# Kernel optimization log

Hardware: AMD Instinct MI355X
Metric: run time of the kernel (lower is better)

Reference implementation:

```python
import jax, jax.numpy as jnp
import numpy as np

N_NODES = 50000
N_EDGES = 800000
N_GRAPHS = 64
NFEAT, NHID, NHEADS, NCLASS = 128, 64, 4, 1
NLAYERS = 3
DT, ALPHA, GAMMA = 1.0, 1.0, 1.0
NEG_SLOPE = 0.2  # PyG GATConv default


def setup_inputs() -> dict:
    key = jax.random.key(0)
    ks = jax.random.split(key, 16)
    HW = NHEADS * NHID
    s = 0.05
    return {
        "x": jax.random.normal(ks[0], (N_NODES, 125), jnp.float32),
        "pos": jax.random.normal(ks[1], (N_NODES, 3), jnp.float32),
        "edge_index": jax.random.randint(ks[2], (2, N_EDGES), 0, N_NODES, jnp.int64),
        "batch": jnp.sort(jax.random.randint(ks[3], (N_NODES,), 0, N_GRAPHS, jnp.int64)),
        "enc_w": jax.random.normal(ks[4], (NFEAT, NHID), jnp.float32) * s,
        "enc_b": jnp.zeros((NHID,), jnp.float32),
        "res_w": jax.random.normal(ks[5], (NHID, HW), jnp.float32) * s,
        "res_b": jnp.zeros((HW,), jnp.float32),
        "lin_w": jax.random.normal(ks[6], (NHID, HW), jnp.float32) * s,
        "att_src": jax.random.normal(ks[7], (NHEADS, NHID), jnp.float32) * s,
        "att_dst": jax.random.normal(ks[8], (NHEADS, NHID), jnp.float32) * s,
        "conv_b": jnp.zeros((HW,), jnp.float32),
        "dec_w": jax.random.normal(ks[9], (NHID, NCLASS), jnp.float32) * s,
        "dec_b": jnp.zeros((NCLASS,), jnp.float32),
    }


def gat_conv(X, src, dst, lin_w, att_src, att_dst, conv_b):
    # X: [N, NHID] -> h: [N, H, C]; per-edge attention, segment softmax over dst, scatter-add
    N = X.shape[0]
    h = (X @ lin_w).reshape(N, NHEADS, NHID)
    a_src = jnp.einsum("nhc,hc->nh", h, att_src)  # [N, H]
    a_dst = jnp.einsum("nhc,hc->nh", h, att_dst)
    e = jax.nn.leaky_relu(a_src[src] + a_dst[dst], NEG_SLOPE)  # [E, H]
    m = jax.ops.segment_max(e, dst, num_segments=N)
    e = jnp.exp(e - m[dst])
    z = jax.ops.segment_sum(e, dst, num_segments=N)
    att = e / z[dst]  # [E, H] (self-loops guarantee z > 0)
    msg = h[src] * att[:, :, None]  # [E, H, C]
    out = jax.ops.segment_sum(msg, dst, num_segments=N)  # [N, H, C]
    return out.reshape(N, NHEADS * NHID) + conv_b


def reference(x, pos, edge_index, batch, enc_w, enc_b, res_w, res_b,
              lin_w, att_src, att_dst, conv_b, dec_w, dec_b):
    inp = jnp.concatenate([x, pos], axis=-1)  # [N, NFEAT]
    N = inp.shape[0]
    loop = jnp.arange(N, dtype=edge_index.dtype)
    src = jnp.concatenate([edge_index[0], loop])  # add self loops (PyG default)
    dst = jnp.concatenate([edge_index[1], loop])

    Y = inp @ enc_w + enc_b
    X = Y
    for _ in range(NLAYERS):
        conv_out = gat_conv(X, src, dst, lin_w, att_src, att_dst, conv_b)
        res = X @ res_w + res_b
        # NB: faithful to torch .view(n, -1, nheads).mean(-1) head-mixing reshape
        mixed = jax.nn.elu(conv_out + res).reshape(N, -1, NHEADS).mean(axis=-1)
        Y = Y + DT * (mixed - ALPHA * Y - GAMMA * X)
        X = X + DT * Y
    X = X @ dec_w + dec_b  # [N, NCLASS]
    pooled = jax.ops.segment_sum(X, batch, num_segments=N_GRAPHS)  # [G, NCLASS]
    return pooled.squeeze(-1)
```

## Files before the change

kernel.cpp:

```cpp
#include <hip/hip_runtime.h>
#include <hip/hip_bf16.h>

#define N_NODES  50000
#define N_EDGES  800000
#define E_TOT    850000
#define N_GRAPHS 64
#define NHID     64
#define NHEADS   4
#define HW       256
#define NEG_SLOPE 0.2f
#define DEC_BLOCKS 512
#define LOG_NPB  32
#define ENC_NPB  32
#define SCAN_NB  ((N_NODES + 255) / 256)
#define MFMA_NPB 64

typedef __attribute__((ext_vector_type(8))) short bf16x8;
typedef __attribute__((ext_vector_type(4))) float f32x4;

__device__ __forceinline__ float bf2f(unsigned short u) {
    return __uint_as_float(((unsigned)u) << 16);
}
__device__ __forceinline__ unsigned short f2bf(float f) {
    __hip_bfloat16 h = __float2bfloat16(f);
    return *reinterpret_cast<unsigned short*>(&h);
}
__device__ __forceinline__ float lrelu(float v) {
    return (v > 0.f) ? v : NEG_SLOPE * v;
}

__global__ __launch_bounds__(256) void encoder_kernel(
        const float* __restrict__ x, const float* __restrict__ pos,
        const float* __restrict__ enc_w, const float* __restrict__ enc_b,
        float* __restrict__ Y, float* __restrict__ X) {
    __shared__ float ws[128 * 64];
    __shared__ float xs[ENC_NPB][128];
    int t = threadIdx.x;
    int base = blockIdx.x * ENC_NPB;
    int nx = min(ENC_NPB, N_NODES - base);
    for (int i = t; i < 128 * 64; i += 256) ws[i] = enc_w[i];
    for (int i = t; i < nx * 125; i += 256) {
        int nn = i / 125, k = i - nn * 125;
        xs[nn][k] = x[(size_t)base * 125 + i];
    }
    for (int i = t; i < nx * 3; i += 256) {
        int nn = i / 3, k = i - nn * 3;
        xs[nn][125 + k] = pos[(size_t)(base + nn) * 3 + k];
    }
    __syncthreads();
    int c = t & 63, wv = t >> 6;
    float bias = enc_b[c];
    for (int nn = wv; nn < nx; nn += 4) {
        float acc = bias;
        #pragma unroll 16
        for (int k = 0; k < 128; ++k) acc += xs[nn][k] * ws[k * 64 + c];
        int n = base + nn;
        Y[n * 64 + c] = acc;
        X[n * 64 + c] = acc;
    }
}

__global__ void hist_kernel(const int* __restrict__ ei, int* __restrict__ counts) {
    int e = blockIdx.x * blockDim.x + threadIdx.x;
    if (e >= E_TOT) return;
    int d = (e < N_EDGES) ? ei[N_EDGES + e] : (e - N_EDGES);
    atomicAdd(&counts[d], 1);
}

__global__ __launch_bounds__(256) void scan_reduce_kernel(const int* __restrict__ counts,
                                                          int* __restrict__ bsum) {
    __shared__ int s[256];
    int t = threadIdx.x;
    int i = blockIdx.x * 256 + t;
    s[t] = (i < N_NODES) ? counts[i] : 0;
    __syncthreads();
    #pragma unroll
    for (int off = 128; off >= 1; off >>= 1) {
        if (t < off) s[t] += s[t + off];
        __syncthreads();
    }
    if (t == 0) bsum[blockIdx.x] = s[0];
}

__global__ __launch_bounds__(256) void scan_bsum_kernel(const int* __restrict__ bsum,
                                                        int* __restrict__ boff) {
    __shared__ int a[256];
    int t = threadIdx.x;
    int v = (t < SCAN_NB) ? bsum[t] : 0;
    a[t] = v;
    __syncthreads();
    #pragma unroll
    for (int off = 1; off < 256; off <<= 1) {
        int u = (t >= off) ? a[t - off] : 0;
        __syncthreads();
        a[t] += u;
        __syncthreads();
    }
    if (t < SCAN_NB) boff[t] = a[t] - v;
}

__global__ __launch_bounds__(256) void scan_write_kernel(const int* __restrict__ counts,
                                                         const int* __restrict__ boff,
                                                         int* __restrict__ row_ptr,
                                                         int* __restrict__ cursor) {
    __shared__ int a[256];
    int t = threadIdx.x;
    int i = blockIdx.x * 256 + t;
    int v = (i < N_NODES) ? counts[i] : 0;
    a[t] = v;
    __syncthreads();
    #pragma unroll
    for (int off = 1; off < 256; off <<= 1) {
        int u = (t >= off) ? a[t - off] : 0;
        __syncthreads();
        a[t] += u;
        __syncthreads();
    }
    if (i < N_NODES) {
        int ex = boff[blockIdx.x] + a[t] - v;
        row_ptr[i] = ex;
        cursor[i]  = ex;
        if (i == N_NODES - 1) row_ptr[N_NODES] = E_TOT;
    }
}

__global__ void scatter_kernel(const int* __restrict__ ei, int* __restrict__ cursor,
                               int* __restrict__ col) {
    int e = blockIdx.x * blockDim.x + threadIdx.x;
    if (e >= E_TOT) return;
    int s, d;
    if (e < N_EDGES) { s = ei[e]; d = ei[N_EDGES + e]; }
    else             { s = d = e - N_EDGES; }
    int pos = atomicAdd(&cursor[d], 1);
    col[pos] = s;
}

__global__ __launch_bounds__(256) void wa_precompute_kernel(
        const float* __restrict__ lin_w, const float* __restrict__ att_src,
        const float* __restrict__ att_dst, float* __restrict__ wa) {
    int t = threadIdx.x;
    int k = t >> 2, head = t & 3;
    float s = 0.f, d = 0.f;
    #pragma unroll 8
    for (int c = 0; c < 64; ++c) {
        float lw = lin_w[k * 256 + head * 64 + c];
        s += lw * att_src[head * 64 + c];
        d += lw * att_dst[head * 64 + c];
    }
    wa[k * 8 + head]     = s;
    wa[k * 8 + 4 + head] = d;
}

__global__ __launch_bounds__(256) void prep_wt_kernel(
        const float* __restrict__ lin_w, const float* __restrict__ res_w,
        unsigned short* __restrict__ Wt) {
    int k = blockIdx.x;
    int t = threadIdx.x;
    Wt[(size_t)t * 64 + k]         = f2bf(lin_w[k * 256 + t]);
    Wt[(size_t)(t + 256) * 64 + k] = f2bf(res_w[k * 256 + t]);
}

__global__ __launch_bounds__(256) void logit_kernel(
        const float* __restrict__ X, const float* __restrict__ wa,
        float* __restrict__ a_src, float* __restrict__ a_dst) {
    __shared__ float was[64 * 8];
    __shared__ float xs[LOG_NPB * 68];
    int t = threadIdx.x;
    int base = blockIdx.x * LOG_NPB;
    int nx = min(LOG_NPB, N_NODES - base);
    for (int i = t; i < 512; i += 256) was[i] = wa[i];
    for (int i = t; i < nx * 64; i += 256)
        xs[(i >> 6) * 68 + (i & 63)] = X[(size_t)base * 64 + i];
    __syncthreads();
    int sub = t >> 3, out = t & 7;
    if (sub >= nx) return;
    float acc = 0.f;
    #pragma unroll 8
    for (int k = 0; k < 64; ++k) acc += xs[sub * 68 + k] * was[k * 8 + out];
    int n = base + sub;
    if (out < 4) a_src[n * 4 + out] = acc;
    else         a_dst[n * 4 + (out - 4)] = acc;
}

__global__ __launch_bounds__(256) void lin_mfma_kernel(
        const float* __restrict__ X, const unsigned short* __restrict__ Wt,
        __hip_bfloat16* __restrict__ h, __hip_bfloat16* __restrict__ res) {
    __shared__ unsigned short As[64 * 64];
    __shared__ unsigned short Bs[256 * 64];
    int t = threadIdx.x;
    int lane = t & 63, w = t >> 6;
    int base = blockIdx.x * MFMA_NPB;

    for (int i = 0; i < 4; ++i) {
        int chunk = i * 256 + t;
        int row = chunk >> 4, q = chunk & 15;
        int node = base + row;
        float4 xv = make_float4(0.f, 0.f, 0.f, 0.f);
        if (node < N_NODES) xv = ((const float4*)X)[(size_t)node * 16 + q];
        ushort4 b;
        b.x = f2bf(xv.x); b.y = f2bf(xv.y); b.z = f2bf(xv.z); b.w = f2bf(xv.w);
        int idx = row * 64 + ((q * 4) ^ ((row & 7) << 3));
        *(ushort4*)&As[idx] = b;
    }

    int rowl = (w << 4) + (lane & 15);
    int kg   = (lane >> 4) << 3;
    int amask = (lane & 7) << 3;
    bf16x8 af0, af1;

    for (int p = 0; p < 2; ++p) {
        __syncthreads();
        const unsigned short* Wp = Wt + (size_t)p * 256 * 64;
        for (int i = 0; i < 8; ++i) {
            int chunk = i * 256 + t;
            int n = chunk >> 3, c = chunk & 7;
            int idx = n * 64 + ((c * 8) ^ ((n & 7) << 3));
            *(uint4*)&Bs[idx] = *(const uint4*)(Wp + chunk * 8);
        }
        __syncthreads();
        if (p == 0) {
            af0 = *(bf16x8*)&As[rowl * 64 + (kg ^ amask)];
            af1 = *(bf16x8*)&As[rowl * 64 + ((32 + kg) ^ amask)];
        }
        for (int ct = 0; ct < 16; ++ct) {
            int coll = (ct << 4) + (lane & 15);
            bf16x8 bf0 = *(bf16x8*)&Bs[coll * 64 + (kg ^ amask)];
            bf16x8 bf1 = *(bf16x8*)&Bs[coll * 64 + ((32 + kg) ^ amask)];
            f32x4 acc = {0.f, 0.f, 0.f, 0.f};
            acc = __builtin_amdgcn_mfma_f32_16x16x32_bf16(af0, bf0, acc, 0, 0, 0);
            acc = __builtin_amdgcn_mfma_f32_16x16x32_bf16(af1, bf1, acc, 0, 0, 0);
            int rowbase = base + (w << 4) + ((lane >> 4) << 2);
            #pragma unroll
            for (int r = 0; r < 4; ++r) {
                int rn = rowbase + r;
                if (rn < N_NODES) {
                    if (p == 0) h[(size_t)rn * 256 + coll] = __float2bfloat16(acc[r]);
                    else        res[(size_t)rn * 256 + coll] = __float2bfloat16(acc[r]);
                }
            }
        }
    }
}

__global__ __launch_bounds__(256) void fused_gat_kernel(
        const int* __restrict__ rp, const int* __restrict__ col,
        const float* __restrict__ a_src, const float* __restrict__ a_dst,
        const __hip_bfloat16* __restrict__ h,
        const float* __restrict__ conv_b,
        const __hip_bfloat16* __restrict__ res,
        float* __restrict__ Y, float* __restrict__ X) {
    __shared__ float satt[4][64][4];
    __shared__ int   scol[4][64];
    int n = (blockIdx.x * blockDim.x + threadIdx.x) >> 6;
    if (n >= N_NODES) return;
    int lane = threadIdx.x & 63;
    int w = (threadIdx.x >> 6) & 3;
    int head = lane >> 4;
    int base = rp[n];
    int deg  = rp[n + 1] - base;
    const ushort* hp = (const ushort*)h;
    float4 ad = ((const float4*)a_dst)[n];

    float a0 = 0.f, a1 = 0.f, a2 = 0.f, a3 = 0.f;

    if (deg <= 64) {
        int s = 0;
        float l0 = -3.0e38f, l1 = -3.0e38f, l2 = -3.0e38f, l3 = -3.0e38f;
        if (lane < deg) {
            s = col[base + lane];
            float4 as = ((const float4*)a_src)[s];
            l0 = lrelu(as.x + ad.x); l1 = lrelu(as.y + ad.y);
            l2 = lrelu(as.z + ad.z); l3 = lrelu(as.w + ad.w);
        }
        float m0 = l0, m1 = l1, m2 = l2, m3 = l3;
        #pragma unroll
        for (int off = 1; off < 64; off <<= 1) {
            m0 = fmaxf(m0, __shfl_xor(m0, off)); m1 = fmaxf(m1, __shfl_xor(m1, off));
            m2 = fmaxf(m2, __shfl_xor(m2, off)); m3 = fmaxf(m3, __shfl_xor(m3, off));
        }
        float e0 = (lane < deg) ? __expf(l0 - m0) : 0.f;
        float e1 = (lane < deg) ? __expf(l1 - m1) : 0.f;
        float e2 = (lane < deg) ? __expf(l2 - m2) : 0.f;
        float e3 = (lane < deg) ? __expf(l3 - m3) : 0.f;
        float z0 = e0, z1 = e1, z2 = e2, z3 = e3;
        #pragma unroll
        for (int off = 1; off < 64; off <<= 1) {
            z0 += __shfl_xor(z0, off); z1 += __shfl_xor(z1, off);
            z2 += __shfl_xor(z2, off); z3 += __shfl_xor(z3, off);
        }
        satt[w][lane][0] = e0 / z0; satt[w][lane][1] = e1 / z1;
        satt[w][lane][2] = e2 / z2; satt[w][lane][3] = e3 / z3;
        scol[w][lane] = s;

        int j = 0;
        for (; j + 2 <= deg; j += 2) {
            int   s0 = scol[w][j],        s1 = scol[w][j + 1];
            float w0 = satt[w][j][head],  w1 = satt[w][j + 1][head];
            ushort4 v0 = *(const ushort4*)(hp + (size_t)s0 * 256 + lane * 4);
            ushort4 v1 = *(const ushort4*)(hp + (size_t)s1 * 256 + lane * 4);
            a0 += w0 * bf2f(v0.x) + w1 * bf2f(v1.x);
            a1 += w0 * bf2f(v0.y) + w1 * bf2f(v1.y);
            a2 += w0 * bf2f(v0.z) + w1 * bf2f(v1.z);
            a3 += w0 * bf2f(v0.w) + w1 * bf2f(v1.w);
        }
        if (j < deg) {
            int   s0 = scol[w][j];
            float w0 = satt[w][j][head];
            ushort4 v0 = *(const ushort4*)(hp + (size_t)s0 * 256 + lane * 4);
            a0 += w0 * bf2f(v0.x); a1 += w0 * bf2f(v0.y);
            a2 += w0 * bf2f(v0.z); a3 += w0 * bf2f(v0.w);
        }
    } else {
        float m0 = -3.0e38f, m1 = -3.0e38f, m2 = -3.0e38f, m3 = -3.0e38f;
        float z0 = 0.f, z1 = 0.f, z2 = 0.f, z3 = 0.f;
        for (int c0 = 0; c0 < deg; c0 += 64) {
            int j = c0 + lane;
            float l0 = -3.0e38f, l1 = -3.0e38f, l2 = -3.0e38f, l3 = -3.0e38f;
            if (j < deg) {
                int s = col[base + j];
                float4 as = ((const float4*)a_src)[s];
                l0 = lrelu(as.x + ad.x); l1 = lrelu(as.y + ad.y);
                l2 = lrelu(as.z + ad.z); l3 = lrelu(as.w + ad.w);
            }
            float c0m = l0, c1m = l1, c2m = l2, c3m = l3;
            #pragma unroll
            for (int off = 1; off < 64; off <<= 1) {
                c0m = fmaxf(c0m, __shfl_xor(c0m, off)); c1m = fmaxf(c1m, __shfl_xor(c1m, off));
                c2m = fmaxf(c2m, __shfl_xor(c2m, off)); c3m = fmaxf(c3m, __shfl_xor(c3m, off));
            }
            float n0 = fmaxf(m0, c0m), n1 = fmaxf(m1, c1m);
            float n2 = fmaxf(m2, c2m), n3 = fmaxf(m3, c3m);
            z0 *= __expf(m0 - n0); z1 *= __expf(m1 - n1);
            z2 *= __expf(m2 - n2); z3 *= __expf(m3 - n3);
            m0 = n0; m1 = n1; m2 = n2; m3 = n3;
            float e0 = (j < deg) ? __expf(l0 - m0) : 0.f;
            float e1 = (j < deg) ? __expf(l1 - m1) : 0.f;
            float e2 = (j < deg) ? __expf(l2 - m2) : 0.f;
            float e3 = (j < deg) ? __expf(l3 - m3) : 0.f;
            #pragma unroll
            for (int off = 1; off < 64; off <<= 1) {
                e0 += __shfl_xor(e0, off); e1 += __shfl_xor(e1, off);
                e2 += __shfl_xor(e2, off); e3 += __shfl_xor(e3, off);
            }
            z0 += e0; z1 += e1; z2 += e2; z3 += e3;
        }
        for (int c0 = 0; c0 < deg; c0 += 64) {
            int j = c0 + lane;
            int s = 0;
            float e0 = 0.f, e1 = 0.f, e2 = 0.f, e3 = 0.f;
            if (j < deg) {
                s = col[base + j];
                float4 as = ((const float4*)a_src)[s];
                e0 = __expf(lrelu(as.x + ad.x) - m0) / z0;
                e1 = __expf(lrelu(as.y + ad.y) - m1) / z1;
                e2 = __expf(lrelu(as.z + ad.z) - m2) / z2;
                e3 = __expf(lrelu(as.w + ad.w) - m3) / z3;
            }
            satt[w][lane][0] = e0; satt[w][lane][1] = e1;
            satt[w][lane][2] = e2; satt[w][lane][3] = e3;
            scol[w][lane] = s;
            int cnt = min(64, deg - c0);
            for (int jj = 0; jj < cnt; ++jj) {
                int   sj = scol[w][jj];
                float ww = satt[w][jj][head];
                ushort4 v = *(const ushort4*)(hp + (size_t)sj * 256 + lane * 4);
                a0 += ww * bf2f(v.x); a1 += ww * bf2f(v.y);
                a2 += ww * bf2f(v.z); a3 += ww * bf2f(v.w);
            }
        }
    }

    ushort4 rr4 = ((const ushort4*)res)[(size_t)n * 64 + lane];
    float4 cb = ((const float4*)conv_b)[lane];
    float v0 = a0 + cb.x + bf2f(rr4.x), v1 = a1 + cb.y + bf2f(rr4.y);
    float v2 = a2 + cb.z + bf2f(rr4.z), v3 = a3 + cb.w + bf2f(rr4.w);
    v0 = (v0 > 0.f) ? v0 : (__expf(v0) - 1.f);
    v1 = (v1 > 0.f) ? v1 : (__expf(v1) - 1.f);
    v2 = (v2 > 0.f) ? v2 : (__expf(v2) - 1.f);
    v3 = (v3 > 0.f) ? v3 : (__expf(v3) - 1.f);
    float mixed = 0.25f * (v0 + v1 + v2 + v3);

    float xv = X[n * 64 + lane];
    float y = Y[n * 64 + lane];
    y  = y + (mixed - y - xv);
    xv = xv + y;
    Y[n * 64 + lane] = y;
    X[n * 64 + lane] = xv;
}

__global__ void decoder_partial_kernel(const float* __restrict__ X, const float* __restrict__ dec_w,
                                       const float* __restrict__ dec_b, const int* __restrict__ batch,
                                       float* __restrict__ partials) {
    __shared__ float sg[N_GRAPHS];
    int t = threadIdx.x;
    if (t < N_GRAPHS) sg[t] = 0.f;
    __syncthreads();
    int lane = t & 63;
    int wave = t >> 6;
    const int npb = (N_NODES + DEC_BLOCKS - 1) / DEC_BLOCKS;
    int start = blockIdx.x * npb;
    int end   = min(start + npb, N_NODES);
    float dw = dec_w[lane];
    float db = dec_b[0];
    for (int n = start + wave; n < end; n += 4) {
        float p = X[n * 64 + lane] * dw;
        #pragma unroll
        for (int off = 32; off >= 1; off >>= 1) p += __shfl_down(p, off);
        if (lane == 0) atomicAdd(&sg[batch[n]], p + db);
    }
    __syncthreads();
    if (t < N_GRAPHS) partials[blockIdx.x * N_GRAPHS + t] = sg[t];
}

__global__ void decoder_reduce_kernel(const float* __restrict__ partials, float* __restrict__ out) {
    __shared__ float red[256];
    int t = threadIdx.x;
    int g = t & 63, j = t >> 6;
    float s = 0.f;
    for (int b = j * (DEC_BLOCKS / 4); b < (j + 1) * (DEC_BLOCKS / 4); ++b)
        s += partials[b * N_GRAPHS + g];
    red[t] = s;
    __syncthreads();
    if (t < 64) out[g] = red[g] + red[64 + g] + red[128 + g] + red[192 + g];
}

extern "C" void kernel_launch(void* const* d_in, const int* in_sizes, int n_in,
                              void* d_out, int out_size, void* d_ws, size_t ws_size,
                              hipStream_t stream) {
    const float* x       = (const float*)d_in[0];
    const float* pos     = (const float*)d_in[1];
    const int*   ei      = (const int*)d_in[2];
    const int*   batch   = (const int*)d_in[3];
    const float* enc_w   = (const float*)d_in[4];
    const float* enc_b   = (const float*)d_in[5];
    const float* res_w   = (const float*)d_in[6];
    const float* res_b   = (const float*)d_in[7];
    const float* lin_w   = (const float*)d_in[8];
    const float* att_src = (const float*)d_in[9];
    const float* att_dst = (const float*)d_in[10];
    const float* conv_b  = (const float*)d_in[11];
    const float* dec_w   = (const float*)d_in[12];
    const float* dec_b   = (const float*)d_in[13];
    float* out = (float*)d_out;

    char* ws = (char*)d_ws;
    size_t off = 0;
    auto alloc = [&](size_t bytes) -> void* {
        void* p = ws + off;
        off += (bytes + 255) & ~size_t(255);
        return p;
    };
    float* Y       = (float*)alloc((size_t)N_NODES * 64 * sizeof(float));
    float* X       = (float*)alloc((size_t)N_NODES * 64 * sizeof(float));
    __hip_bfloat16* h   = (__hip_bfloat16*)alloc((size_t)N_NODES * HW * sizeof(__hip_bfloat16));
    __hip_bfloat16* res = (__hip_bfloat16*)alloc((size_t)N_NODES * HW * sizeof(__hip_bfloat16));
    float* a_src   = (float*)alloc((size_t)N_NODES * NHEADS * sizeof(float));
    float* a_dst   = (float*)alloc((size_t)N_NODES * NHEADS * sizeof(float));
    float* wa      = (float*)alloc((size_t)64 * 8 * sizeof(float));
    unsigned short* Wt = (unsigned short*)alloc((size_t)512 * 64 * sizeof(unsigned short));
    float* partials= (float*)alloc((size_t)DEC_BLOCKS * N_GRAPHS * sizeof(float));
    int*   counts  = (int*)alloc((size_t)N_NODES * sizeof(int));
    int*   row_ptr = (int*)alloc((size_t)(N_NODES + 1) * sizeof(int));
    int*   cursor  = (int*)alloc((size_t)N_NODES * sizeof(int));
    int*   col     = (int*)alloc((size_t)E_TOT * sizeof(int));
    int*   bsum    = (int*)alloc((size_t)SCAN_NB * sizeof(int));
    int*   boff    = (int*)alloc((size_t)SCAN_NB * sizeof(int));

    hipMemsetAsync(counts, 0, (size_t)N_NODES * sizeof(int), stream);
    const int eb = (E_TOT + 255) / 256;
    hist_kernel<<<eb, 256, 0, stream>>>(ei, counts);
    scan_reduce_kernel<<<SCAN_NB, 256, 0, stream>>>(counts, bsum);
    scan_bsum_kernel<<<1, 256, 0, stream>>>(bsum, boff);
    scan_write_kernel<<<SCAN_NB, 256, 0, stream>>>(counts, boff, row_ptr, cursor);
    scatter_kernel<<<eb, 256, 0, stream>>>(ei, cursor, col);

    wa_precompute_kernel<<<1, 256, 0, stream>>>(lin_w, att_src, att_dst, wa);
    prep_wt_kernel<<<64, 256, 0, stream>>>(lin_w, res_w, Wt);
    encoder_kernel<<<(N_NODES + ENC_NPB - 1) / ENC_NPB, 256, 0, stream>>>(
        x, pos, enc_w, enc_b, Y, X);

    const int ab = (N_NODES * 64 + 255) / 256;
    const int mb = (N_NODES + MFMA_NPB - 1) / MFMA_NPB;
    const int gb = (N_NODES + LOG_NPB - 1) / LOG_NPB;
    for (int layer = 0; layer < 3; ++layer) {
        lin_mfma_kernel<<<mb, 256, 0, stream>>>(X, Wt, h, res);
        logit_kernel<<<gb, 256, 0, stream>>>(X, wa, a_src, a_dst);
        fused_gat_kernel<<<ab, 256, 0, stream>>>(row_ptr, col, a_src, a_dst, h,
                                                 conv_b, res, Y, X);
    }

    decoder_partial_kernel<<<DEC_BLOCKS, 256, 0, stream>>>(X, dec_w, dec_b, batch, partials);
    decoder_reduce_kernel<<<1, 256, 0, stream>>>(partials, out);
}
```

Measured before the change: 527.4 us.

## Fuse attention logit projection into MFMA linear kernel and unroll gather by four

```diff
diff --git a/kernel.cpp b/kernel.cpp
--- a/kernel.cpp
+++ b/kernel.cpp
@@ -10,7 +10,6 @@
 #define HW       256
 #define NEG_SLOPE 0.2f
 #define DEC_BLOCKS 512
-#define LOG_NPB  32
 #define ENC_NPB  32
 #define SCAN_NB  ((N_NODES + 255) / 256)
 #define MFMA_NPB 64
@@ -137,7 +136,7 @@
 
 __global__ __launch_bounds__(256) void wa_precompute_kernel(
         const float* __restrict__ lin_w, const float* __restrict__ att_src,
-        const float* __restrict__ att_dst, float* __restrict__ wa) {
+        const float* __restrict__ att_dst, unsigned short* __restrict__ Wt) {
     int t = threadIdx.x;
     int k = t >> 2, head = t & 3;
     float s = 0.f, d = 0.f;
@@ -147,8 +146,10 @@
         s += lw * att_src[head * 64 + c];
         d += lw * att_dst[head * 64 + c];
     }
-    wa[k * 8 + head]     = s;
-    wa[k * 8 + 4 + head] = d;
+    Wt[(size_t)(512 + head) * 64 + k] = f2bf(s);
+    Wt[(size_t)(516 + head) * 64 + k] = f2bf(d);
+    Wt[(size_t)520 * 64 + t]       = 0;
+    Wt[(size_t)520 * 64 + 256 + t] = 0;
 }
 
 __global__ __launch_bounds__(256) void prep_wt_kernel(
@@ -160,31 +161,10 @@
     Wt[(size_t)(t + 256) * 64 + k] = f2bf(res_w[k * 256 + t]);
 }
 
-__global__ __launch_bounds__(256) void logit_kernel(
-        const float* __restrict__ X, const float* __restrict__ wa,
-        float* __restrict__ a_src, float* __restrict__ a_dst) {
-    __shared__ float was[64 * 8];
-    __shared__ float xs[LOG_NPB * 68];
-    int t = threadIdx.x;
-    int base = blockIdx.x * LOG_NPB;
-    int nx = min(LOG_NPB, N_NODES - base);
-    for (int i = t; i < 512; i += 256) was[i] = wa[i];
-    for (int i = t; i < nx * 64; i += 256)
-        xs[(i >> 6) * 68 + (i & 63)] = X[(size_t)base * 64 + i];
-    __syncthreads();
-    int sub = t >> 3, out = t & 7;
-    if (sub >= nx) return;
-    float acc = 0.f;
-    #pragma unroll 8
-    for (int k = 0; k < 64; ++k) acc += xs[sub * 68 + k] * was[k * 8 + out];
-    int n = base + sub;
-    if (out < 4) a_src[n * 4 + out] = acc;
-    else         a_dst[n * 4 + (out - 4)] = acc;
-}
-
 __global__ __launch_bounds__(256) void lin_mfma_kernel(
         const float* __restrict__ X, const unsigned short* __restrict__ Wt,
-        __hip_bfloat16* __restrict__ h, __hip_bfloat16* __restrict__ res) {
+        __hip_bfloat16* __restrict__ h, __hip_bfloat16* __restrict__ res,
+        float* __restrict__ a_src, float* __restrict__ a_dst) {
     __shared__ unsigned short As[64 * 64];
     __shared__ unsigned short Bs[256 * 64];
     int t = threadIdx.x;
@@ -216,6 +196,11 @@
             int n = chunk >> 3, c = chunk & 7;
             int idx = n * 64 + ((c * 8) ^ ((n & 7) << 3));
             *(uint4*)&Bs[idx] = *(const uint4*)(Wp + chunk * 8);
+        }
+        if (p == 1 && t < 128) {
+            int n = t >> 3, c = t & 7;
+            int idx = n * 64 + ((c * 8) ^ ((n & 7) << 3));
+            *(uint4*)&As[idx] = *(const uint4*)(Wt + (size_t)(512 + n) * 64 + c * 8);
         }
         __syncthreads();
         if (p == 0) {
@@ -236,6 +221,23 @@
                 if (rn < N_NODES) {
                     if (p == 0) h[(size_t)rn * 256 + coll] = __float2bfloat16(acc[r]);
                     else        res[(size_t)rn * 256 + coll] = __float2bfloat16(acc[r]);
+                }
+            }
+        }
+        if (p == 1) {
+            int coll = lane & 15;
+            bf16x8 bf0 = *(bf16x8*)&As[coll * 64 + (kg ^ amask)];
+            bf16x8 bf1 = *(bf16x8*)&As[coll * 64 + ((32 + kg) ^ amask)];
+            f32x4 acc = {0.f, 0.f, 0.f, 0.f};
+            acc = __builtin_amdgcn_mfma_f32_16x16x32_bf16(af0, bf0, acc, 0, 0, 0);
+            acc = __builtin_amdgcn_mfma_f32_16x16x32_bf16(af1, bf1, acc, 0, 0, 0);
+            int rowbase = base + (w << 4) + ((lane >> 4) << 2);
+            #pragma unroll
+            for (int r = 0; r < 4; ++r) {
+                int rn = rowbase + r;
+                if (rn < N_NODES) {
+                    if (coll < 4)      a_src[rn * 4 + coll] = acc[r];
+                    else if (coll < 8) a_dst[rn * 4 + (coll - 4)] = acc[r];
                 }
             }
         }
@@ -293,17 +295,21 @@
         scol[w][lane] = s;
 
         int j = 0;
-        for (; j + 2 <= deg; j += 2) {
-            int   s0 = scol[w][j],        s1 = scol[w][j + 1];
-            float w0 = satt[w][j][head],  w1 = satt[w][j + 1][head];
+        for (; j + 4 <= deg; j += 4) {
+            int   s0 = scol[w][j],       s1 = scol[w][j + 1];
+            int   s2 = scol[w][j + 2],   s3 = scol[w][j + 3];
+            float w0 = satt[w][j][head], w1 = satt[w][j + 1][head];
+            float w2 = satt[w][j + 2][head], w3 = satt[w][j + 3][head];
             ushort4 v0 = *(const ushort4*)(hp + (size_t)s0 * 256 + lane * 4);
             ushort4 v1 = *(const ushort4*)(hp + (size_t)s1 * 256 + lane * 4);
-            a0 += w0 * bf2f(v0.x) + w1 * bf2f(v1.x);
-            a1 += w0 * bf2f(v0.y) + w1 * bf2f(v1.y);
-            a2 += w0 * bf2f(v0.z) + w1 * bf2f(v1.z);
-            a3 += w0 * bf2f(v0.w) + w1 * bf2f(v1.w);
-        }
-        if (j < deg) {
+            ushort4 v2 = *(const ushort4*)(hp + (size_t)s2 * 256 + lane * 4);
+            ushort4 v3 = *(const ushort4*)(hp + (size_t)s3 * 256 + lane * 4);
+            a0 += w0 * bf2f(v0.x) + w1 * bf2f(v1.x) + w2 * bf2f(v2.x) + w3 * bf2f(v3.x);
+            a1 += w0 * bf2f(v0.y) + w1 * bf2f(v1.y) + w2 * bf2f(v2.y) + w3 * bf2f(v3.y);
+            a2 += w0 * bf2f(v0.z) + w1 * bf2f(v1.z) + w2 * bf2f(v2.z) + w3 * bf2f(v3.z);
+            a3 += w0 * bf2f(v0.w) + w1 * bf2f(v1.w) + w2 * bf2f(v2.w) + w3 * bf2f(v3.w);
+        }
+        for (; j < deg; ++j) {
             int   s0 = scol[w][j];
             float w0 = satt[w][j][head];
             ushort4 v0 = *(const ushort4*)(hp + (size_t)s0 * 256 + lane * 4);
@@ -456,8 +462,7 @@
     __hip_bfloat16* res = (__hip_bfloat16*)alloc((size_t)N_NODES * HW * sizeof(__hip_bfloat16));
     float* a_src   = (float*)alloc((size_t)N_NODES * NHEADS * sizeof(float));
     float* a_dst   = (float*)alloc((size_t)N_NODES * NHEADS * sizeof(float));
-    float* wa      = (float*)alloc((size_t)64 * 8 * sizeof(float));
-    unsigned short* Wt = (unsigned short*)alloc((size_t)512 * 64 * sizeof(unsigned short));
+    unsigned short* Wt = (unsigned short*)alloc((size_t)528 * 64 * sizeof(unsigned short));
     float* partials= (float*)alloc((size_t)DEC_BLOCKS * N_GRAPHS * sizeof(float));
     int*   counts  = (int*)alloc((size_t)N_NODES * sizeof(int));
     int*   row_ptr = (int*)alloc((size_t)(N_NODES + 1) * sizeof(int));
@@ -474,17 +479,15 @@
     scan_write_kernel<<<SCAN_NB, 256, 0, stream>>>(counts, boff, row_ptr, cursor);
     scatter_kernel<<<eb, 256, 0, stream>>>(ei, cursor, col);
 
-    wa_precompute_kernel<<<1, 256, 0, stream>>>(lin_w, att_src, att_dst, wa);
+    wa_precompute_kernel<<<1, 256, 0, stream>>>(lin_w, att_src, att_dst, Wt);
     prep_wt_kernel<<<64, 256, 0, stream>>>(lin_w, res_w, Wt);
     encoder_kernel<<<(N_NODES + ENC_NPB - 1) / ENC_NPB, 256, 0, stream>>>(
         x, pos, enc_w, enc_b, Y, X);
 
     const int ab = (N_NODES * 64 + 255) / 256;
     const int mb = (N_NODES + MFMA_NPB - 1) / MFMA_NPB;
-    const int gb = (N_NODES + LOG_NPB - 1) / LOG_NPB;
     for (int layer = 0; layer < 3; ++layer) {
-        lin_mfma_kernel<<<mb, 256, 0, stream>>>(X, Wt, h, res);
-        logit_kernel<<<gb, 256, 0, stream>>>(X, wa, a_src, a_dst);
+        lin_mfma_kernel<<<mb, 256, 0, stream>>>(X, Wt, h, res, a_src, a_dst);
         fused_gat_kernel<<<ab, 256, 0, stream>>>(row_ptr, col, a_src, a_dst, h,
                                                  conv_b, res, Y, X);
     }
```

After: 501.9 us. 1.05x faster.
